# Optimization experiments

Measured on AMD Instinct MI355X. Metric: run time of the kernel, lower is better.

## Reference

```python
import jax, jax.numpy as jnp
import numpy as np

B, T, E, H = 4, 2048, 1024, 16
D = E // H
SCALE = 1.0 / np.sqrt(D)


def setup_inputs() -> dict:
    key = jax.random.key(0)
    ks = jax.random.split(key, 5)
    s_in = 1.0 / np.sqrt(E)
    return {
        "x": jax.random.normal(ks[0], (B, T, E), dtype=jnp.float32),
        "W_qkv": jax.random.normal(ks[1], (E, 3 * E), dtype=jnp.float32) * s_in,
        "b_qkv": jax.random.normal(ks[2], (3 * E,), dtype=jnp.float32) * 0.02,
        "W_proj": jax.random.normal(ks[3], (E, E), dtype=jnp.float32) * s_in,
        "b_proj": jax.random.normal(ks[4], (E,), dtype=jnp.float32) * 0.02,
    }


def reference(x, W_qkv, b_qkv, W_proj, b_proj):
    Bx, Tx, _ = x.shape
    qkv = x @ W_qkv + b_qkv                      # [B, T, 3E]
    q, k, v = jnp.split(qkv, 3, axis=2)
    q = q.reshape(Bx, Tx, H, D)
    k = k.reshape(Bx, Tx, H, D)
    v = v.reshape(Bx, Tx, H, D)
    # scores [B, H, T, T]
    a = SCALE * jnp.einsum("bthd,bshd->bhts", q, k)
    causal = jnp.tril(jnp.ones((Tx, Tx), dtype=bool))
    a = jnp.where(causal, a, -jnp.inf)
    a = jax.nn.softmax(a, axis=-1)
    y = jnp.einsum("bhts,bshd->bthd", a, v).reshape(Bx, Tx, E)
    return y @ W_proj + b_proj
```

## Files before the change

kernel.cpp:

```cpp
#include <hip/hip_runtime.h>
#include <math.h>

#define Bn 4
#define Tn 2048
#define En 1024
#define Hn 16
#define Dn 64
#define RS2 (2 * En)
#define QSCALE 0.18033688f
#define SMAX 16.0f

typedef __attribute__((ext_vector_type(8))) short bfrag;
typedef __attribute__((ext_vector_type(4))) short sfrag4;
typedef __attribute__((ext_vector_type(4))) float ffrag;

__device__ __forceinline__ unsigned short f2bf(float f) {
    union { float f; unsigned int u; } v; v.f = f;
    unsigned int r = v.u + 0x7fffu + ((v.u >> 16) & 1u);
    return (unsigned short)(r >> 16);
}
__device__ __forceinline__ unsigned short f2bf_fast(float f) {
    union { float f; unsigned int u; } v; v.f = f;
    return (unsigned short)((v.u + 0x8000u) >> 16);
}

__device__ __forceinline__ void glds16(const unsigned short* g, unsigned short* l) {
    __builtin_amdgcn_global_load_lds(
        (const __attribute__((address_space(1))) unsigned int*)g,
        (__attribute__((address_space(3))) unsigned int*)l, 16, 0, 0);
}

__global__ __launch_bounds__(256) void f2bf_vec(const float* __restrict__ in,
                                                unsigned short* __restrict__ out, int n) {
    int i = (blockIdx.x * 256 + threadIdx.x) * 4;
    if (i >= n) return;
    float4 v = *(const float4*)(in + i);
    ushort4 o;
    o.x = f2bf(v.x); o.y = f2bf(v.y); o.z = f2bf(v.z); o.w = f2bf(v.w);
    *(ushort4*)(out + i) = o;
}

__global__ __launch_bounds__(256) void transpose_f2bf(const float* __restrict__ W,
                                                      unsigned short* __restrict__ Wt,
                                                      int K, int N) {
    __shared__ float s[64][65];
    const int kt = blockIdx.y * 64, nt = blockIdx.x * 64;
    const int tx = threadIdx.x & 15, ty = threadIdx.x >> 4;
#pragma unroll
    for (int i = 0; i < 4; ++i) {
        float4 v = *(const float4*)&W[(size_t)(kt + ty + i * 16) * N + nt + tx * 4];
        s[ty + i * 16][tx * 4 + 0] = v.x;
        s[ty + i * 16][tx * 4 + 1] = v.y;
        s[ty + i * 16][tx * 4 + 2] = v.z;
        s[ty + i * 16][tx * 4 + 3] = v.w;
    }
    __syncthreads();
#pragma unroll
    for (int i = 0; i < 4; ++i) {
        const int n = ty + i * 16;
        ushort4 o;
        o.x = f2bf(s[tx * 4 + 0][n]);
        o.y = f2bf(s[tx * 4 + 1][n]);
        o.z = f2bf(s[tx * 4 + 2][n]);
        o.w = f2bf(s[tx * 4 + 3][n]);
        *(ushort4*)&Wt[(size_t)(nt + n) * K + kt + tx * 4] = o;
    }
}

template <int OUT_BF16, int VSPLIT>
__global__ __launch_bounds__(256) void gemm_nt_mfma(
    const unsigned short* __restrict__ A, const unsigned short* __restrict__ Bt,
    const float* __restrict__ bias, void* __restrict__ Cv, int ldc,
    unsigned short* __restrict__ vt, int vstart,
    int M, int N, int K, int qcols, int gx)
{
    __shared__ __attribute__((aligned(16))) unsigned short As[128 * 64];
    __shared__ __attribute__((aligned(16))) unsigned short Bs[128 * 64];

    const int t = threadIdx.x;
    const int w = t >> 6, l = t & 63;
    const int wmt = (w & 1) * 4, wnt = (w >> 1) * 4;
    const int nl = l & 15, lq = l >> 4;
    const int r8 = l >> 3, c8 = l & 7;
    const int cs8 = c8 ^ r8;

    const int flat = blockIdx.x;
    const int xcd = flat & 7;
    const int g = flat >> 3;
    const int bx = g % gx;
    const int by = xcd * 8 + g / gx;
    const int m0 = by * 128, n0 = bx * 128;

    ffrag acc[4][4];
#pragma unroll
    for (int i = 0; i < 4; ++i)
#pragma unroll
        for (int j = 0; j < 4; ++j)
#pragma unroll
            for (int r = 0; r < 4; ++r) acc[i][j][r] = 0.f;

    const unsigned short* Ag = A  + (size_t)(m0 + r8) * K + cs8 * 8;
    const unsigned short* Bg = Bt + (size_t)(n0 + r8) * K + cs8 * 8;

    const int iters = K >> 6;
#pragma unroll 1
    for (int it = 0; it < iters; ++it) {
        const int k0 = it << 6;
        __syncthreads();
#pragma unroll
        for (int r = 0; r < 4; ++r) {
            const int i = w * 4 + r;
            glds16(Ag + (size_t)(i * 8) * K + k0, &As[i * 512 + l * 8]);
            glds16(Bg + (size_t)(i * 8) * K + k0, &Bs[i * 512 + l * 8]);
        }
        __syncthreads();
#pragma unroll
        for (int ks = 0; ks < 2; ++ks) {
            bfrag af[4], bf[4];
#pragma unroll
            for (int i = 0; i < 4; ++i) {
                const int pos = ((ks * 4 + lq) ^ (nl & 7)) << 3;
                af[i] = *(const bfrag*)&As[((wmt + i) * 16 + nl) * 64 + pos];
                bf[i] = *(const bfrag*)&Bs[((wnt + i) * 16 + nl) * 64 + pos];
            }
#pragma unroll
            for (int i = 0; i < 4; ++i)
#pragma unroll
                for (int j = 0; j < 4; ++j)
                    acc[i][j] = __builtin_amdgcn_mfma_f32_16x16x32_bf16(af[i], bf[j], acc[i][j], 0, 0, 0);
        }
    }

    const int orow = lq * 4, ocol = nl;
#pragma unroll
    for (int i = 0; i < 4; ++i) {
        const int gm = m0 + (wmt + i) * 16 + orow;
#pragma unroll
        for (int j = 0; j < 4; ++j) {
            const int gn = n0 + (wnt + j) * 16 + ocol;
            const float bs = bias[gn];
            if (VSPLIT && gn >= vstart) {
                const int vc = gn - vstart;
                const int b  = gm / Tn;
                const int tt = gm - b * Tn;
                ushort4 o;
                o.x = f2bf(acc[i][j][0] + bs);
                o.y = f2bf(acc[i][j][1] + bs);
                o.z = f2bf(acc[i][j][2] + bs);
                o.w = f2bf(acc[i][j][3] + bs);
                *(ushort4*)&vt[(size_t)(b * Hn * Dn + vc) * Tn + tt] = o;
            } else {
                const float sc = (qcols && gn < qcols) ? QSCALE : 1.f;
#pragma unroll
                for (int r = 0; r < 4; ++r) {
                    const float vv = (acc[i][j][r] + bs) * sc;
                    if (OUT_BF16)
                        ((unsigned short*)Cv)[(size_t)(gm + r) * ldc + gn] = f2bf(vv);
                    else
                        ((float*)Cv)[(size_t)(gm + r) * ldc + gn] = vv;
                }
            }
        }
    }
}

__global__ __launch_bounds__(256, 4) void attn_mfma(
    const unsigned short* __restrict__ qkv,
    const unsigned short* __restrict__ vtg,
    unsigned short* __restrict__ yattn)
{
    __shared__ __attribute__((aligned(16))) unsigned short KT[128 * 64];
    __shared__ __attribute__((aligned(16))) unsigned short VT[64 * 128];

    const int t = threadIdx.x;
    const int w = t >> 6, l = t & 63;
    const int nl = l & 15, lq = l >> 4;
    const int flat = blockIdx.x;
    const int bh = flat & 63;
    const int qp = flat >> 6;
    const int b = bh >> 4, h = bh & 15;

    const unsigned short* qbase = qkv + (size_t)(b * Tn) * RS2 + h * Dn;
    const unsigned short* kbase = qbase + En;
    const unsigned short* vbase = vtg + (size_t)(bh * Dn) * Tn;
    unsigned short* yb = yattn + (size_t)(b * Tn) * En + h * Dn;

#pragma unroll 1
    for (int phase = 0; phase < 2; ++phase) {
        const int qt = phase ? (31 - qp) : qp;
        const int rowb = qt * 64 + w * 16;
        const int jmax = qt >> 1;
        const int qrow = rowb + nl;

        bfrag qf[2];
#pragma unroll
        for (int ks = 0; ks < 2; ++ks)
            qf[ks] = *(const bfrag*)(qbase + (size_t)(rowb + nl) * RS2 + ks * 32 + lq * 8);

        ffrag Oa[4];
        float li = 0.f;
#pragma unroll
        for (int dt = 0; dt < 4; ++dt)
#pragma unroll
            for (int r = 0; r < 4; ++r) Oa[dt][r] = 0.f;

        for (int j = 0; j <= jmax; ++j) {
            const int k0 = j << 7;
            __syncthreads();
#pragma unroll
            for (int r = 0; r < 4; ++r) {
                const int i = w * 4 + r;
                glds16(kbase + (size_t)(k0 + i * 8 + (l >> 3)) * RS2 + (((l & 7) ^ (l >> 3)) << 3),
                       &KT[i * 512 + l * 8]);
            }
#pragma unroll
            for (int r = 0; r < 4; ++r) {
                const int i = w * 4 + r;
                const int key = ((i & 3) << 2) + (l >> 4);
                glds16(vbase + (size_t)(i * 4 + (l >> 4)) * Tn + k0 + (((l & 15) ^ key) << 3),
                       &VT[i * 512 + l * 8]);
            }
            __syncthreads();

            bfrag pf[4];
#pragma unroll
            for (int cs = 0; cs < 4; ++cs) {
                const int n0 = cs * 2, n1 = cs * 2 + 1;
                const int pos0 = (lq ^ (nl & 7)) << 3;
                const int pos1 = ((4 + lq) ^ (nl & 7)) << 3;
                bfrag ka0 = *(const bfrag*)&KT[(n0 * 16 + nl) * 64 + pos0];
                bfrag kb0 = *(const bfrag*)&KT[(n0 * 16 + nl) * 64 + pos1];
                bfrag ka1 = *(const bfrag*)&KT[(n1 * 16 + nl) * 64 + pos0];
                bfrag kb1 = *(const bfrag*)&KT[(n1 * 16 + nl) * 64 + pos1];
                ffrag z0, z1;
#pragma unroll
                for (int r = 0; r < 4; ++r) { z0[r] = -SMAX; z1[r] = -SMAX; }
                __builtin_amdgcn_s_setprio(1);
                z0 = __builtin_amdgcn_mfma_f32_16x16x32_bf16(ka0, qf[0], z0, 0, 0, 0);
                z0 = __builtin_amdgcn_mfma_f32_16x16x32_bf16(kb0, qf[1], z0, 0, 0, 0);
                z1 = __builtin_amdgcn_mfma_f32_16x16x32_bf16(ka1, qf[0], z1, 0, 0, 0);
                z1 = __builtin_amdgcn_mfma_f32_16x16x32_bf16(kb1, qf[1], z1, 0, 0, 0);
                __builtin_amdgcn_s_setprio(0);
                if (j == jmax) {
#pragma unroll
                    for (int r = 0; r < 4; ++r) {
                        if (k0 + n0 * 16 + lq * 4 + r > qrow) z0[r] = -INFINITY;
                        if (k0 + n1 * 16 + lq * 4 + r > qrow) z1[r] = -INFINITY;
                    }
                }
#pragma unroll
                for (int r = 0; r < 4; ++r) {
                    const float p0 = __builtin_amdgcn_exp2f(z0[r]);
                    const float p1 = __builtin_amdgcn_exp2f(z1[r]);
                    li += p0;
                    li += p1;
                    pf[cs][r]     = (short)f2bf_fast(p0);
                    pf[cs][4 + r] = (short)f2bf_fast(p1);
                }
            }

            __builtin_amdgcn_s_setprio(1);
#pragma unroll
            for (int cs = 0; cs < 4; ++cs) {
#pragma unroll
                for (int dt = 0; dt < 4; ++dt) {
                    const int d = dt * 16 + nl;
                    const int base = d * 128 + ((lq & 1) << 2);
                    const int cA = (((cs << 2) + (lq >> 1)) ^ nl) << 3;
                    const int cB = (((cs << 2) + 2 + (lq >> 1)) ^ nl) << 3;
                    sfrag4 va = *(const sfrag4*)&VT[base + cA];
                    sfrag4 vb = *(const sfrag4*)&VT[base + cB];
                    bfrag vf = __builtin_shufflevector(va, vb, 0, 1, 2, 3, 4, 5, 6, 7);
                    Oa[dt] = __builtin_amdgcn_mfma_f32_16x16x32_bf16(pf[cs], vf, Oa[dt], 0, 0, 0);
                }
            }
            __builtin_amdgcn_s_setprio(0);
        }

        li += __shfl_xor(li, 16, 64);
        li += __shfl_xor(li, 32, 64);
#pragma unroll
        for (int r = 0; r < 4; ++r) {
            const float lr = __shfl(li, lq * 4 + r, 64);
            const float inv = 1.f / lr;
            const int row = rowb + lq * 4 + r;
#pragma unroll
            for (int dt = 0; dt < 4; ++dt)
                yb[(size_t)row * En + dt * 16 + nl] = f2bf(Oa[dt][r] * inv);
        }
    }
}

extern "C" void kernel_launch(void* const* d_in, const int* in_sizes, int n_in,
                              void* d_out, int out_size, void* d_ws, size_t ws_size,
                              hipStream_t stream)
{
    const float* x      = (const float*)d_in[0];
    const float* W_qkv  = (const float*)d_in[1];
    const float* b_qkv  = (const float*)d_in[2];
    const float* W_proj = (const float*)d_in[3];
    const float* b_proj = (const float*)d_in[4];
    float* out = (float*)d_out;

    const int M = Bn * Tn;
    char* ws = (char*)d_ws;
    unsigned short* xb   = (unsigned short*)ws; ws += (size_t)M * En * 2;
    unsigned short* Wqt  = (unsigned short*)ws; ws += (size_t)3 * En * En * 2;
    unsigned short* Wpt  = (unsigned short*)ws; ws += (size_t)En * En * 2;
    unsigned short* qkb  = (unsigned short*)ws; ws += (size_t)M * 2 * En * 2;
    unsigned short* vtg  = (unsigned short*)ws; ws += (size_t)M * En * 2;
    unsigned short* yb   = (unsigned short*)ws;

    f2bf_vec<<<(M * En / 4 + 255) / 256, 256, 0, stream>>>(x, xb, M * En);
    transpose_f2bf<<<dim3(3 * En / 64, En / 64), 256, 0, stream>>>(W_qkv, Wqt, En, 3 * En);
    transpose_f2bf<<<dim3(En / 64, En / 64), 256, 0, stream>>>(W_proj, Wpt, En, En);

    gemm_nt_mfma<1, 1><<<dim3((3 * En / 128) * (M / 128)), 256, 0, stream>>>(
        xb, Wqt, b_qkv, qkb, 2 * En, vtg, 2 * En, M, 3 * En, En, En, 3 * En / 128);

    attn_mfma<<<dim3(1024), 256, 0, stream>>>(qkb, vtg, yb);

    gemm_nt_mfma<0, 0><<<dim3((En / 128) * (M / 128)), 256, 0, stream>>>(
        yb, Wpt, b_proj, out, En, nullptr, 1 << 30, M, En, En, 0, En / 128);
}
```

Before: 255.4 us.

## Add 256x256-tile double-buffered QKV GEMM with interleaved staging and MFMA quarters

Replaces the QKV projection's 128x128-tile GEMM with a dedicated 512-thread kernel computing 256x256 output tiles, double-buffering 64-wide K slices in LDS via direct global-to-LDS loads with XOR swizzle. Each K step is split into four MFMA quarters interleaved with the next tile's staging, using explicit vmcnt waits, barriers and setprio to overlap memory and compute. Block index remapping groups tiles for L2 reuse. The larger tile raises arithmetic intensity but uses 128KB LDS and one block per CU, with 384 blocks covering 256 CUs unevenly.

```diff
diff --git a/kernel.cpp b/kernel.cpp
--- a/kernel.cpp
+++ b/kernel.cpp
@@ -29,6 +29,11 @@
         (const __attribute__((address_space(1))) unsigned int*)g,
         (__attribute__((address_space(3))) unsigned int*)l, 16, 0, 0);
 }
+
+#define VMCNT(n) asm volatile("s_waitcnt vmcnt(" #n ")" ::: "memory")
+#define LGKM0()  do { asm volatile("s_waitcnt lgkmcnt(0)" ::: "memory"); \
+                      __builtin_amdgcn_sched_barrier(0); } while (0)
+#define BAR()    __builtin_amdgcn_s_barrier()
 
 __global__ __launch_bounds__(256) void f2bf_vec(const float* __restrict__ in,
                                                 unsigned short* __restrict__ out, int n) {
@@ -164,6 +169,156 @@
     }
 }
 
+__global__ __launch_bounds__(512, 1) void gemm_qkv_256(
+    const unsigned short* __restrict__ A,
+    const unsigned short* __restrict__ Bt,
+    const float* __restrict__ bias,
+    unsigned short* __restrict__ qk,
+    unsigned short* __restrict__ vt)
+{
+    __shared__ __attribute__((aligned(16))) unsigned short As[2][256 * 64];
+    __shared__ __attribute__((aligned(16))) unsigned short Bs[2][256 * 64];
+
+    const int t = threadIdx.x;
+    const int w = t >> 6, l = t & 63;
+    const int wm16 = (w & 1) << 4, wn16 = (w >> 1) << 4;
+    const int nl = l & 15, lq = l >> 4, nl7 = l & 7;
+    const int r8 = l >> 3, c8 = l & 7;
+    const int cs8 = c8 ^ r8;
+
+    const int flat = blockIdx.x;
+    const int g = flat >> 3;
+    const int bx = g % 12;
+    const int by = (flat & 7) * 4 + g / 12;
+    const int m0 = by << 8, n0 = bx << 8;
+
+    ffrag acc[8][4];
+#pragma unroll
+    for (int i = 0; i < 8; ++i)
+#pragma unroll
+        for (int j = 0; j < 4; ++j)
+#pragma unroll
+            for (int r = 0; r < 4; ++r) acc[i][j][r] = 0.f;
+
+    const unsigned short* Ag = A  + (size_t)(m0 + r8) * 1024 + cs8 * 8;
+    const unsigned short* Bg = Bt + (size_t)(n0 + r8) * 1024 + cs8 * 8;
+
+#define STAGE_A(goff, kofs, dst)                                                      \
+    _Pragma("unroll")                                                                 \
+    for (int s = 0; s < 2; ++s) {                                                     \
+        const int gg = (goff) + w * 2 + s;                                            \
+        glds16(Ag + (size_t)(gg * 8) * 1024 + (kofs), (dst) + gg * 512 + l * 8);      \
+    }
+#define STAGE_B(goff, kofs, dst)                                                      \
+    _Pragma("unroll")                                                                 \
+    for (int s = 0; s < 2; ++s) {                                                     \
+        const int gg = (goff) + w * 2 + s;                                            \
+        glds16(Bg + (size_t)(gg * 8) * 1024 + (kofs), (dst) + gg * 512 + l * 8);      \
+    }
+#define LOAD_A(MH)                                                                    \
+    _Pragma("unroll")                                                                 \
+    for (int ks = 0; ks < 2; ++ks)                                                    \
+        _Pragma("unroll")                                                             \
+        for (int i = 0; i < 4; ++i)                                                   \
+            af[ks][i] = *(const bfrag*)&Asc[(((MH) * 4 + i) * 32 + wm16 + nl) * 64 +  \
+                                            (((ks * 4 + lq) ^ nl7) << 3)];
+#define LOAD_B(NH)                                                                    \
+    _Pragma("unroll")                                                                 \
+    for (int ks = 0; ks < 2; ++ks)                                                    \
+        _Pragma("unroll")                                                             \
+        for (int j = 0; j < 2; ++j)                                                   \
+            bf[ks][j] = *(const bfrag*)&Bsc[(((NH) * 2 + j) * 64 + wn16 + nl) * 64 +  \
+                                            (((ks * 4 + lq) ^ nl7) << 3)];
+#define MFMA_Q(MH, NH)                                                                \
+    __builtin_amdgcn_s_setprio(1);                                                    \
+    _Pragma("unroll")                                                                 \
+    for (int ks = 0; ks < 2; ++ks)                                                    \
+        _Pragma("unroll")                                                             \
+        for (int i = 0; i < 4; ++i)                                                   \
+            _Pragma("unroll")                                                         \
+            for (int j = 0; j < 2; ++j)                                               \
+                acc[(MH) * 4 + i][(NH) * 2 + j] = __builtin_amdgcn_mfma_f32_16x16x32_bf16( \
+                    af[ks][i], bf[ks][j], acc[(MH) * 4 + i][(NH) * 2 + j], 0, 0, 0);  \
+    __builtin_amdgcn_s_setprio(0);
+
+    STAGE_A(0, 0, &As[0][0]);
+    STAGE_B(0, 0, &Bs[0][0]);
+    STAGE_B(16, 0, &Bs[0][0]);
+    STAGE_A(16, 0, &As[0][0]);
+    VMCNT(4);
+    BAR();
+
+#pragma unroll 1
+    for (int it = 0; it < 16; ++it) {
+        const int buf = it & 1;
+        const size_t kn = (size_t)(it + 1) << 6;
+        const bool more = it < 15;
+        const unsigned short* Asc = &As[buf][0];
+        const unsigned short* Bsc = &Bs[buf][0];
+        unsigned short* Asn = &As[buf ^ 1][0];
+        unsigned short* Bsn = &Bs[buf ^ 1][0];
+        bfrag af[2][4], bf[2][2];
+
+        LOAD_A(0);
+        LOAD_B(0);
+        if (more) { STAGE_A(0, kn, Asn); VMCNT(4); } else { VMCNT(2); }
+        BAR(); LGKM0();
+        MFMA_Q(0, 0);
+        BAR();
+
+        LOAD_B(1);
+        if (more) { STAGE_B(0, kn, Bsn); VMCNT(4); } else { VMCNT(0); }
+        BAR(); LGKM0();
+        MFMA_Q(0, 1);
+        BAR();
+
+        LOAD_A(1);
+        if (more) { STAGE_B(16, kn, Bsn); VMCNT(2); }
+        BAR(); LGKM0();
+        MFMA_Q(1, 1);
+        BAR();
+
+        LOAD_B(0);
+        if (more) { STAGE_A(16, kn, Asn); }
+        BAR(); LGKM0();
+        MFMA_Q(1, 0);
+        BAR();
+    }
+
+#undef STAGE_A
+#undef STAGE_B
+#undef LOAD_A
+#undef LOAD_B
+#undef MFMA_Q
+
+    const int orow = lq * 4;
+#pragma unroll
+    for (int i = 0; i < 8; ++i) {
+        const int gm = m0 + i * 32 + wm16 + orow;
+#pragma unroll
+        for (int j = 0; j < 4; ++j) {
+            const int gn = n0 + j * 64 + wn16 + nl;
+            const float bs = bias[gn];
+            if (gn >= 2 * En) {
+                const int vc = gn - 2 * En;
+                const int b  = gm >> 11;
+                const int tt = gm & (Tn - 1);
+                ushort4 o;
+                o.x = f2bf(acc[i][j][0] + bs);
+                o.y = f2bf(acc[i][j][1] + bs);
+                o.z = f2bf(acc[i][j][2] + bs);
+                o.w = f2bf(acc[i][j][3] + bs);
+                *(ushort4*)&vt[(size_t)(b * Hn * Dn + vc) * Tn + tt] = o;
+            } else {
+                const float sc = (gn < En) ? QSCALE : 1.f;
+#pragma unroll
+                for (int r = 0; r < 4; ++r)
+                    qk[(size_t)(gm + r) * RS2 + gn] = f2bf((acc[i][j][r] + bs) * sc);
+            }
+        }
+    }
+}
+
 __global__ __launch_bounds__(256, 4) void attn_mfma(
     const unsigned short* __restrict__ qkv,
     const unsigned short* __restrict__ vtg,
@@ -315,8 +470,7 @@
     transpose_f2bf<<<dim3(3 * En / 64, En / 64), 256, 0, stream>>>(W_qkv, Wqt, En, 3 * En);
     transpose_f2bf<<<dim3(En / 64, En / 64), 256, 0, stream>>>(W_proj, Wpt, En, En);
 
-    gemm_nt_mfma<1, 1><<<dim3((3 * En / 128) * (M / 128)), 256, 0, stream>>>(
-        xb, Wqt, b_qkv, qkb, 2 * En, vtg, 2 * En, M, 3 * En, En, En, 3 * En / 128);
+    gemm_qkv_256<<<dim3(384), 512, 0, stream>>>(xb, Wqt, b_qkv, qkb, vtg);
 
     attn_mfma<<<dim3(1024), 256, 0, stream>>>(qkb, vtg, yb);
 
```

After: 255.8 us. About the same (+0.1%).
